# Kernel tuning notes

Hardware: AMD Instinct MI355X
Metric: run time of the kernel (lower is better)

The kernel has to match this reference:

```python
import jax, jax.numpy as jnp
import numpy as np

NEG_SLOPE = 0.2
EPS = 1e-16
HEADS1, OUT1 = 4, 32
HEADS2, OUT2 = 1, 32


def _gat_conv(x, W, a_src, a_dst, bias, src, dst, num_nodes, heads, out_c, concat):
    # x: [N, F_in], W: [F_in, heads*out_c], a_*: [heads, out_c]
    h = (x @ W).reshape(num_nodes, heads, out_c)            # [N, H, C]
    alpha_src = (h * a_src).sum(-1)                          # [N, H]
    alpha_dst = (h * a_dst).sum(-1)                          # [N, H]
    e = jax.nn.leaky_relu(alpha_src[src] + alpha_dst[dst], NEG_SLOPE)  # [E, H]
    # softmax over incoming edges of each destination node (PyG softmax)
    m = jax.ops.segment_max(e, dst, num_segments=num_nodes)
    ex = jnp.exp(e - m[dst])
    s = jax.ops.segment_sum(ex, dst, num_segments=num_nodes)
    alpha = ex / (s[dst] + EPS)                              # [E, H]
    out = jax.ops.segment_sum(h[src] * alpha[:, :, None], dst,
                              num_segments=num_nodes)        # [N, H, C]
    out = out.reshape(num_nodes, heads * out_c) if concat else out.mean(axis=1)
    return out + bias


def setup_inputs() -> dict:
    key = jax.random.key(0)
    ks = jax.random.split(key, 10)
    N, E, F_IN = 50000, 1600000, 128
    sc = 0.1
    return {
        "x": jax.random.normal(ks[0], (N, F_IN), jnp.float32),
        "edge_index": jax.random.randint(ks[1], (2, E), 0, N, jnp.int32),
        "W1": jax.random.normal(ks[2], (F_IN, HEADS1 * OUT1), jnp.float32) * sc,
        "a_src1": jax.random.normal(ks[3], (HEADS1, OUT1), jnp.float32) * sc,
        "a_dst1": jax.random.normal(ks[4], (HEADS1, OUT1), jnp.float32) * sc,
        "b1": jax.random.normal(ks[5], (HEADS1 * OUT1,), jnp.float32) * sc,
        "W2": jax.random.normal(ks[6], (HEADS1 * OUT1, HEADS2 * OUT2), jnp.float32) * sc,
        "a_src2": jax.random.normal(ks[7], (HEADS2, OUT2), jnp.float32) * sc,
        "a_dst2": jax.random.normal(ks[8], (HEADS2, OUT2), jnp.float32) * sc,
        "b2": jax.random.normal(ks[9], (OUT2,), jnp.float32) * sc,
    }


def reference(x, edge_index, W1, a_src1, a_dst1, b1, W2, a_src2, a_dst2, b2):
    N = x.shape[0]
    # PyG GATConv default add_self_loops=True
    loops = jnp.arange(N, dtype=edge_index.dtype)
    src = jnp.concatenate([edge_index[0], loops])
    dst = jnp.concatenate([edge_index[1], loops])
    h = _gat_conv(x, W1, a_src1, a_dst1, b1, src, dst, N, HEADS1, OUT1, True)
    h = jax.nn.elu(h)
    return _gat_conv(h, W2, a_src2, a_dst2, b2, src, dst, N, HEADS2, OUT2, False)
```

## Files before the change

### kernel.cpp

```cpp
#include <hip/hip_runtime.h>
#include <math.h>

#define NEG_SLOPE 0.2f
#define EPSV 1e-16f
#define NPART 4

typedef _Float16 half4 __attribute__((ext_vector_type(4)));
typedef _Float16 half8 __attribute__((ext_vector_type(8)));
typedef float floatx2 __attribute__((ext_vector_type(2)));


__global__ void k_scan_blk(const int* __restrict__ degp, int N,
                           int* __restrict__ rowptr, int* __restrict__ bsum){
    int b = blockIdx.x, t = threadIdx.x;
    int base = b * 1024 + t * 4;
    int v[4];
    #pragma unroll
    for (int j = 0; j < 4; j++){
        int n = base + j, s = 0;
        if (n < N){
            #pragma unroll
            for (int p = 0; p < NPART; p++) s += degp[p * N + n];
        }
        v[j] = s;
    }
    int s = v[0] + v[1] + v[2] + v[3];
    int lane = t & 63, wid = t >> 6;
    int x = s;
    #pragma unroll
    for (int off = 1; off < 64; off <<= 1){
        int y = __shfl_up(x, off, 64);
        if (lane >= off) x += y;
    }
    __shared__ int ws[4];
    if (lane == 63) ws[wid] = x;
    __syncthreads();
    int woff = 0;
    for (int w = 0; w < wid; w++) woff += ws[w];
    int run = woff + x - s;
    #pragma unroll
    for (int j = 0; j < 4; j++){
        if (base + j < N) rowptr[base + j] = run;
        run += v[j];
    }
    if (t == 255) bsum[b] = woff + x;
}

__global__ void k_finalize(const int* __restrict__ bsum, const int* __restrict__ degp,
                           int N, int ET,
                           int* __restrict__ rowptr, int* __restrict__ poff){
    int b = blockIdx.x, t = threadIdx.x;
    int n = b * 256 + t;
    int chunk = (b * 256) >> 10;
    int off = 0;
    for (int c = 0; c < chunk; c++) off += bsum[c];
    if (n < N){
        int r = rowptr[n] + off;
        rowptr[n] = r;
        int run = r;
        #pragma unroll
        for (int p = 0; p < NPART; p++){
            poff[p * N + n] = run;
            run += degp[p * N + n];
        }
    }
    if (n == 0) rowptr[N] = ET;
}

__launch_bounds__(256)
__global__ void k_scatter2(const int* __restrict__ ei, int E, int ET, int N,
                           const int* __restrict__ poff,
                           const unsigned short* __restrict__ rank,
                           int* __restrict__ csr_src){
    int i = blockIdx.x * 256 + threadIdx.x;
    if (i >= ET) return;
    int s, d;
    if (i < E){ s = ei[i]; d = ei[E + i]; } else { s = i - E; d = s; }
    int p = (i >> 8) & (NPART - 1);
    csr_src[poff[p * N + d] + (int)rank[i]] = s;
}


__launch_bounds__(256)
__global__ void k_gemm1_hist(const float* __restrict__ x, const float* __restrict__ W1,
                             const float* __restrict__ a_src, const float* __restrict__ a_dst,
                             _Float16* __restrict__ h1h, float* __restrict__ asrc1,
                             float* __restrict__ adst1, int N, int nGemmBlk,
                             const int* __restrict__ ei, int E, int ET,
                             int* __restrict__ degp, unsigned short* __restrict__ rank){
    __shared__ float Wl[16 * 128];
    __shared__ float xl[32 * 128];
    int t = threadIdx.x;
    if ((int)blockIdx.x >= nGemmBlk){
        int base = (blockIdx.x - nGemmBlk) * 1024 + t;
        #pragma unroll
        for (int j = 0; j < 4; j++){
            int i = base + j * 256;
            if (i < ET){
                int d = (i < E) ? ei[E + i] : (i - E);
                int p = (i >> 8) & (NPART - 1);
                rank[i] = (unsigned short)atomicAdd(&degp[p * N + d], 1);
            }
        }
        return;
    }
    int cg = t & 31, ns = t >> 5;
    int n0 = blockIdx.x * 32;
    for (int idx = t; idx < 1024; idx += 256){
        int row = idx >> 5, k4 = idx & 31;
        float4 v = {0.f, 0.f, 0.f, 0.f};
        if (n0 + row < N) v = *(const float4*)&x[(size_t)(n0 + row) * 128 + k4 * 4];
        *(float4*)&xl[row * 128 + k4 * 4] = v;
    }
    float4 acc0 = {0,0,0,0}, acc1 = {0,0,0,0}, acc2 = {0,0,0,0}, acc3 = {0,0,0,0};
    for (int c = 0; c < 8; c++){
        __syncthreads();
        for (int idx = t; idx < 512; idx += 256)
            *(float4*)&Wl[idx * 4] = *(const float4*)&W1[c * 16 * 128 + idx * 4];
        __syncthreads();
        #pragma unroll
        for (int k = 0; k < 16; k += 4){
            float4 xv0 = *(float4*)&xl[(ns     ) * 128 + c * 16 + k];
            float4 xv1 = *(float4*)&xl[(ns +  8) * 128 + c * 16 + k];
            float4 xv2 = *(float4*)&xl[(ns + 16) * 128 + c * 16 + k];
            float4 xv3 = *(float4*)&xl[(ns + 24) * 128 + c * 16 + k];
            #pragma unroll
            for (int kk = 0; kk < 4; kk++){
                float4 w = *(float4*)&Wl[(k + kk) * 128 + cg * 4];
                float x0 = ((float*)&xv0)[kk];
                float x1 = ((float*)&xv1)[kk];
                float x2v= ((float*)&xv2)[kk];
                float x3 = ((float*)&xv3)[kk];
                acc0.x = fmaf(x0, w.x, acc0.x); acc0.y = fmaf(x0, w.y, acc0.y);
                acc0.z = fmaf(x0, w.z, acc0.z); acc0.w = fmaf(x0, w.w, acc0.w);
                acc1.x = fmaf(x1, w.x, acc1.x); acc1.y = fmaf(x1, w.y, acc1.y);
                acc1.z = fmaf(x1, w.z, acc1.z); acc1.w = fmaf(x1, w.w, acc1.w);
                acc2.x = fmaf(x2v, w.x, acc2.x); acc2.y = fmaf(x2v, w.y, acc2.y);
                acc2.z = fmaf(x2v, w.z, acc2.z); acc2.w = fmaf(x2v, w.w, acc2.w);
                acc3.x = fmaf(x3, w.x, acc3.x); acc3.y = fmaf(x3, w.y, acc3.y);
                acc3.z = fmaf(x3, w.z, acc3.z); acc3.w = fmaf(x3, w.w, acc3.w);
            }
        }
    }
    float4 a4s = *(const float4*)&a_src[cg * 4];
    float4 a4d = *(const float4*)&a_dst[cg * 4];
    float4 accs[4] = {acc0, acc1, acc2, acc3};
    #pragma unroll
    for (int j = 0; j < 4; j++){
        int n = n0 + ns + 8 * j;
        if (n >= N) continue;
        float4 a = accs[j];
        half4 hv;
        hv.x = (_Float16)a.x; hv.y = (_Float16)a.y;
        hv.z = (_Float16)a.z; hv.w = (_Float16)a.w;
        *(half4*)&h1h[((size_t)n << 7) + (cg << 2)] = hv;
        float vs = a.x * a4s.x + a.y * a4s.y + a.z * a4s.z + a.w * a4s.w;
        float vd = a.x * a4d.x + a.y * a4d.y + a.z * a4d.z + a.w * a4d.w;
        #pragma unroll
        for (int m = 1; m <= 4; m <<= 1){
            vs += __shfl_xor(vs, m, 64);
            vd += __shfl_xor(vd, m, 64);
        }
        if ((cg & 7) == 0){
            int head = cg >> 3;
            asrc1[n * 4 + head] = vs;
            adst1[n * 4 + head] = vd;
        }
    }
}


__launch_bounds__(256)
__global__ void k_agg1(const int* __restrict__ rowptr, const int* __restrict__ csr_src,
                       const float* __restrict__ asrc1, const float* __restrict__ adst1,
                       const _Float16* __restrict__ h1h,
                       const float* __restrict__ b1, float* __restrict__ x2){
    int t = threadIdx.x;
    int n = blockIdx.x * 4 + (t >> 6);
    int lane = t & 63, g = lane >> 4, l = lane & 15, head = l >> 2;
    int start = rowptr[n], end = rowptr[n + 1];
    float adn = adst1[(n << 2) + head];
    const char* hb = (const char*)h1h;
    const char* ab = (const char*)asrc1;
    int hoff = l << 4;
    int aoff = head << 2;
    floatx2 rA[4], rB[4];
    #pragma unroll
    for (int j = 0; j < 4; j++){ rA[j] = (floatx2)0.f; rB[j] = (floatx2)0.f; }
    float sA = 0.f, sB = 0.f;
    int i = start + g;
    for (; i + 4 < end; i += 8){
        int s0 = csr_src[i];
        int s1 = csr_src[i + 4];
        float e0 = *(const float*)(ab + (s0 << 4) + aoff) + adn;
        float e1 = *(const float*)(ab + (s1 << 4) + aoff) + adn;
        e0 = fmaxf(e0, NEG_SLOPE * e0);
        e1 = fmaxf(e1, NEG_SLOPE * e1);
        float w0 = __expf(e0);
        float w1 = __expf(e1);
        half8 h0 = *(const half8*)(hb + (s0 << 8) + hoff);
        half8 h1v = *(const half8*)(hb + (s1 << 8) + hoff);
        sA += w0; sB += w1;
        floatx2 w02 = {w0, w0}, w12 = {w1, w1};
        #pragma unroll
        for (int j = 0; j < 4; j++){
            floatx2 c0 = {(float)h0[2*j], (float)h0[2*j+1]};
            floatx2 c1 = {(float)h1v[2*j], (float)h1v[2*j+1]};
            rA[j] = w02 * c0 + rA[j];
            rB[j] = w12 * c1 + rB[j];
        }
    }
    if (i < end){
        int s0 = csr_src[i];
        float e0 = *(const float*)(ab + (s0 << 4) + aoff) + adn;
        e0 = fmaxf(e0, NEG_SLOPE * e0);
        float w0 = __expf(e0);
        half8 h0 = *(const half8*)(hb + (s0 << 8) + hoff);
        sA += w0;
        floatx2 w02 = {w0, w0};
        #pragma unroll
        for (int j = 0; j < 4; j++){
            floatx2 c0 = {(float)h0[2*j], (float)h0[2*j+1]};
            rA[j] = w02 * c0 + rA[j];
        }
    }
    float r[9];
    #pragma unroll
    for (int j = 0; j < 4; j++){
        floatx2 c = rA[j] + rB[j];
        r[2*j] = c.x; r[2*j+1] = c.y;
    }
    r[8] = sA + sB;
    #pragma unroll
    for (int m = 16; m <= 32; m <<= 1)
        #pragma unroll
        for (int j = 0; j < 9; j++) r[j] += __shfl_xor(r[j], m, 64);
    if (g == 0){
        float inv = 1.f / (r[8] + EPSV);
        float o[8];
        #pragma unroll
        for (int j = 0; j < 8; j++){
            float v = r[j] * inv + b1[l * 8 + j];
            o[j] = (v > 0.f) ? v : expm1f(v);
        }
        float4 o0 = {o[0], o[1], o[2], o[3]};
        float4 o1 = {o[4], o[5], o[6], o[7]};
        *(float4*)&x2[((size_t)n << 7) + (l << 3)]     = o0;
        *(float4*)&x2[((size_t)n << 7) + (l << 3) + 4] = o1;
    }
}


__launch_bounds__(256)
__global__ void k_gemm2(const float* __restrict__ x2, const float* __restrict__ W2,
                        const float* __restrict__ a_src, const float* __restrict__ a_dst,
                        _Float16* __restrict__ h2h, float* __restrict__ asrc2,
                        float* __restrict__ adst2, int N){
    __shared__ float Wl[128 * 32];
    __shared__ float xl[64 * 128];
    int t = threadIdx.x;
    int cg = t & 7, ns = t >> 3;
    for (int idx = t; idx < 1024; idx += 256)
        *(float4*)&Wl[idx * 4] = *(const float4*)&W2[idx * 4];
    int n0 = blockIdx.x * 64;
    for (int idx = t; idx < 2048; idx += 256){
        int row = idx >> 5, k4 = idx & 31;
        float4 v = {0.f, 0.f, 0.f, 0.f};
        if (n0 + row < N) v = *(const float4*)&x2[(size_t)(n0 + row) * 128 + k4 * 4];
        *(float4*)&xl[row * 128 + k4 * 4] = v;
    }
    __syncthreads();
    float4 acc0 = {0,0,0,0}, acc1 = {0,0,0,0};
    #pragma unroll 2
    for (int k = 0; k < 128; k += 4){
        float4 xv0 = *(float4*)&xl[(ns      ) * 128 + k];
        float4 xv1 = *(float4*)&xl[(ns + 32) * 128 + k];
        #pragma unroll
        for (int kk = 0; kk < 4; kk++){
            float4 w = *(float4*)&Wl[(k + kk) * 32 + cg * 4];
            float x0 = ((float*)&xv0)[kk];
            float x1 = ((float*)&xv1)[kk];
            acc0.x = fmaf(x0, w.x, acc0.x); acc0.y = fmaf(x0, w.y, acc0.y);
            acc0.z = fmaf(x0, w.z, acc0.z); acc0.w = fmaf(x0, w.w, acc0.w);
            acc1.x = fmaf(x1, w.x, acc1.x); acc1.y = fmaf(x1, w.y, acc1.y);
            acc1.z = fmaf(x1, w.z, acc1.z); acc1.w = fmaf(x1, w.w, acc1.w);
        }
    }
    float4 a4s = *(const float4*)&a_src[cg * 4];
    float4 a4d = *(const float4*)&a_dst[cg * 4];
    float4 accs[2] = {acc0, acc1};
    #pragma unroll
    for (int j = 0; j < 2; j++){
        int n = n0 + ns + 32 * j;
        if (n >= N) continue;
        float4 a = accs[j];
        half4 hv;
        hv.x = (_Float16)a.x; hv.y = (_Float16)a.y;
        hv.z = (_Float16)a.z; hv.w = (_Float16)a.w;
        *(half4*)&h2h[((size_t)n << 5) + (cg << 2)] = hv;
        float vs = a.x * a4s.x + a.y * a4s.y + a.z * a4s.z + a.w * a4s.w;
        float vd = a.x * a4d.x + a.y * a4d.y + a.z * a4d.z + a.w * a4d.w;
        #pragma unroll
        for (int m = 1; m <= 4; m <<= 1){
            vs += __shfl_xor(vs, m, 64);
            vd += __shfl_xor(vd, m, 64);
        }
        if (cg == 0){ asrc2[n] = vs; adst2[n] = vd; }
    }
}


__launch_bounds__(256)
__global__ void k_agg2(const int* __restrict__ rowptr, const int* __restrict__ csr_src,
                       const float* __restrict__ asrc2, const float* __restrict__ adst2,
                       const _Float16* __restrict__ h2h,
                       const float* __restrict__ b2, float* __restrict__ out){
    int t = threadIdx.x;
    int n = blockIdx.x * 8 + (t >> 5);
    int l5 = t & 31, g = l5 >> 3, l = l5 & 7;
    int start = rowptr[n], end = rowptr[n + 1];
    float adn = adst2[n];
    const char* hb = (const char*)h2h;
    const char* ab = (const char*)asrc2;
    int hoff = l << 3;
    floatx2 aA[2], aB[2];
    aA[0] = (floatx2)0.f; aA[1] = (floatx2)0.f;
    aB[0] = (floatx2)0.f; aB[1] = (floatx2)0.f;
    float sA = 0.f, sB = 0.f;
    int i = start + g;
    for (; i + 4 < end; i += 8){
        int s0 = csr_src[i];
        int s1 = csr_src[i + 4];
        float e0 = *(const float*)(ab + (s0 << 2)) + adn;
        float e1 = *(const float*)(ab + (s1 << 2)) + adn;
        e0 = fmaxf(e0, NEG_SLOPE * e0);
        e1 = fmaxf(e1, NEG_SLOPE * e1);
        float w0 = __expf(e0);
        float w1 = __expf(e1);
        half4 h0 = *(const half4*)(hb + (s0 << 6) + hoff);
        half4 h1v = *(const half4*)(hb + (s1 << 6) + hoff);
        sA += w0; sB += w1;
        floatx2 w02 = {w0, w0}, w12 = {w1, w1};
        floatx2 c00 = {(float)h0.x, (float)h0.y}, c01 = {(float)h0.z, (float)h0.w};
        floatx2 c10 = {(float)h1v.x, (float)h1v.y}, c11 = {(float)h1v.z, (float)h1v.w};
        aA[0] = w02 * c00 + aA[0]; aA[1] = w02 * c01 + aA[1];
        aB[0] = w12 * c10 + aB[0]; aB[1] = w12 * c11 + aB[1];
    }
    if (i < end){
        int s0 = csr_src[i];
        float e0 = *(const float*)(ab + (s0 << 2)) + adn;
        e0 = fmaxf(e0, NEG_SLOPE * e0);
        float w0 = __expf(e0);
        half4 h0 = *(const half4*)(hb + (s0 << 6) + hoff);
        sA += w0;
        floatx2 w02 = {w0, w0};
        floatx2 c00 = {(float)h0.x, (float)h0.y}, c01 = {(float)h0.z, (float)h0.w};
        aA[0] = w02 * c00 + aA[0]; aA[1] = w02 * c01 + aA[1];
    }
    floatx2 m0 = aA[0] + aB[0], m1 = aA[1] + aB[1];
    float4 acc = {m0.x, m0.y, m1.x, m1.y};
    float ssum = sA + sB;
    #pragma unroll
    for (int m = 8; m <= 16; m <<= 1){
        acc.x += __shfl_xor(acc.x, m, 64);
        acc.y += __shfl_xor(acc.y, m, 64);
        acc.z += __shfl_xor(acc.z, m, 64);
        acc.w += __shfl_xor(acc.w, m, 64);
        ssum  += __shfl_xor(ssum,  m, 64);
    }
    if (g == 0){
        float inv = 1.f / (ssum + EPSV);
        const float4 b4 = *(const float4*)&b2[l * 4];
        float4 o;
        o.x = acc.x * inv + b4.x; o.y = acc.y * inv + b4.y;
        o.z = acc.z * inv + b4.z; o.w = acc.w * inv + b4.w;
        *(float4*)&out[((size_t)n << 5) + l * 4] = o;
    }
}


extern "C" void kernel_launch(void* const* d_in, const int* in_sizes, int n_in,
                              void* d_out, int out_size, void* d_ws, size_t ws_size,
                              hipStream_t stream){
    const float* x      = (const float*)d_in[0];
    const int*   ei     = (const int*)  d_in[1];
    const float* W1     = (const float*)d_in[2];
    const float* a_src1 = (const float*)d_in[3];
    const float* a_dst1 = (const float*)d_in[4];
    const float* b1     = (const float*)d_in[5];
    const float* W2     = (const float*)d_in[6];
    const float* a_src2 = (const float*)d_in[7];
    const float* a_dst2 = (const float*)d_in[8];
    const float* b2     = (const float*)d_in[9];
    float* out = (float*)d_out;

    int N  = in_sizes[0] / 128;
    int E  = in_sizes[1] / 2;
    int ET = E + N;
    int nScanBlk = (N + 1023) / 1024;
    int G  = (ET + 255) / 256;
    int GH = (ET + 1023) / 1024;
    int nGemmBlk = (N + 31) / 32;

    char* ws = (char*)d_ws;
    size_t off = 0;
    auto alloc = [&](size_t bytes) -> char* {
        char* p = ws + off;
        off += (bytes + 255) & ~(size_t)255;
        return p;
    };
    int*            degp    = (int*)           alloc((size_t)NPART * N * 4);
    int*            rowptr  = (int*)           alloc((size_t)(N + 1) * 4);
    int*            bsum    = (int*)           alloc((size_t)nScanBlk * 4);
    unsigned short* rank    = (unsigned short*)alloc((size_t)ET * 2);
    int*            poff    = (int*)           alloc((size_t)NPART * N * 4);
    int*            csr_src = (int*)           alloc((size_t)ET * 4);
    _Float16*       h1h     = (_Float16*)      alloc((size_t)N * 128 * 2);
    float*          x2      = (float*)         alloc((size_t)N * 128 * 4);
    float*          asrc1   = (float*)         alloc((size_t)N * 4 * 4);
    float*          adst1   = (float*)         alloc((size_t)N * 4 * 4);
    _Float16*       h2h     = (_Float16*)      alloc((size_t)N * 32 * 2);
    float*          asrc2   = (float*)         alloc((size_t)N * 4);
    float*          adst2   = (float*)         alloc((size_t)N * 4);

    hipMemsetAsync(degp, 0, (size_t)NPART * N * 4, stream);
    hipLaunchKernelGGL(k_gemm1_hist, dim3(nGemmBlk + GH), dim3(256), 0, stream,
                       x, W1, a_src1, a_dst1, h1h, asrc1, adst1, N, nGemmBlk,
                       ei, E, ET, degp, rank);
    hipLaunchKernelGGL(k_scan_blk,  dim3(nScanBlk), dim3(256), 0, stream, degp, N, rowptr, bsum);
    hipLaunchKernelGGL(k_finalize,  dim3((N + 255) / 256), dim3(256), 0, stream, bsum, degp, N, ET, rowptr, poff);
    hipLaunchKernelGGL(k_scatter2,  dim3(G), dim3(256), 0, stream, ei, E, ET, N, poff, rank, csr_src);
    hipLaunchKernelGGL(k_agg1,      dim3(N / 4), dim3(256), 0, stream, rowptr, csr_src, asrc1, adst1, h1h, b1, x2);
    hipLaunchKernelGGL(k_gemm2,     dim3((N + 63) / 64), dim3(256), 0, stream, x2, W2, a_src2, a_dst2, h2h, asrc2, adst2, N);
    hipLaunchKernelGGL(k_agg2,      dim3(N / 8), dim3(256), 0, stream, rowptr, csr_src, asrc2, adst2, h2h, b2, out);
}
```

Baseline: 303.8 us.

## Partition degree histogram by XCC, enlarge GEMM1 tile and keep W in registers

The degree-histogram atomics now pick their partition from the hardware XCC id read via s_getreg, with NPART raised to 8. The partition is packed into the high bits of the 16-bit rank so the scatter can recover it, which limits per-partition degree to 8191. The atomics use workgroup scope, relying on each partition being touched only from one XCC. GEMM1 now computes 64 rows per block with 8 accumulators and loads W1 straight from global into registers instead of staging it in LDS, dropping the per-chunk barriers. The goal is less cross-die atomic contention and fewer LDS round trips, at the cost of higher register pressure.

```diff
diff --git a/kernel.cpp b/kernel.cpp
--- a/kernel.cpp
+++ b/kernel.cpp
@@ -3,7 +3,7 @@
 
 #define NEG_SLOPE 0.2f
 #define EPSV 1e-16f
-#define NPART 4
+#define NPART 8
 
 typedef _Float16 half4 __attribute__((ext_vector_type(4)));
 typedef _Float16 half8 __attribute__((ext_vector_type(8)));
@@ -76,80 +76,80 @@
     if (i >= ET) return;
     int s, d;
     if (i < E){ s = ei[i]; d = ei[E + i]; } else { s = i - E; d = s; }
-    int p = (i >> 8) & (NPART - 1);
-    csr_src[poff[p * N + d] + (int)rank[i]] = s;
-}
-
-
-__launch_bounds__(256)
+    int pr = rank[i];
+    int p = pr >> 13, r = pr & 0x1FFF;
+    csr_src[poff[p * N + d] + r] = s;
+}
+
+
+__launch_bounds__(256, 3)
 __global__ void k_gemm1_hist(const float* __restrict__ x, const float* __restrict__ W1,
                              const float* __restrict__ a_src, const float* __restrict__ a_dst,
                              _Float16* __restrict__ h1h, float* __restrict__ asrc1,
                              float* __restrict__ adst1, int N, int nGemmBlk,
                              const int* __restrict__ ei, int E, int ET,
-                             int* __restrict__ degp, unsigned short* __restrict__ rank){
-    __shared__ float Wl[16 * 128];
-    __shared__ float xl[32 * 128];
+                             unsigned int* __restrict__ degp, unsigned short* __restrict__ rank){
+    __shared__ float xl[64 * 128];
     int t = threadIdx.x;
     if ((int)blockIdx.x >= nGemmBlk){
+        int p = __builtin_amdgcn_s_getreg((3 << 11) | 20) & 7;
         int base = (blockIdx.x - nGemmBlk) * 1024 + t;
         #pragma unroll
         for (int j = 0; j < 4; j++){
             int i = base + j * 256;
             if (i < ET){
                 int d = (i < E) ? ei[E + i] : (i - E);
-                int p = (i >> 8) & (NPART - 1);
-                rank[i] = (unsigned short)atomicAdd(&degp[p * N + d], 1);
+                unsigned r = __hip_atomic_fetch_add(&degp[(size_t)p * N + d], 1u,
+                                 __ATOMIC_RELAXED, __HIP_MEMORY_SCOPE_WORKGROUP);
+                rank[i] = (unsigned short)((p << 13) | r);
             }
         }
         return;
     }
-    int cg = t & 31, ns = t >> 5;
-    int n0 = blockIdx.x * 32;
-    for (int idx = t; idx < 1024; idx += 256){
+    int cg = t & 31, rs = t >> 5;
+    int n0 = blockIdx.x * 64;
+    for (int idx = t; idx < 2048; idx += 256){
         int row = idx >> 5, k4 = idx & 31;
         float4 v = {0.f, 0.f, 0.f, 0.f};
         if (n0 + row < N) v = *(const float4*)&x[(size_t)(n0 + row) * 128 + k4 * 4];
         *(float4*)&xl[row * 128 + k4 * 4] = v;
     }
-    float4 acc0 = {0,0,0,0}, acc1 = {0,0,0,0}, acc2 = {0,0,0,0}, acc3 = {0,0,0,0};
-    for (int c = 0; c < 8; c++){
-        __syncthreads();
-        for (int idx = t; idx < 512; idx += 256)
-            *(float4*)&Wl[idx * 4] = *(const float4*)&W1[c * 16 * 128 + idx * 4];
-        __syncthreads();
-        #pragma unroll
-        for (int k = 0; k < 16; k += 4){
-            float4 xv0 = *(float4*)&xl[(ns     ) * 128 + c * 16 + k];
-            float4 xv1 = *(float4*)&xl[(ns +  8) * 128 + c * 16 + k];
-            float4 xv2 = *(float4*)&xl[(ns + 16) * 128 + c * 16 + k];
-            float4 xv3 = *(float4*)&xl[(ns + 24) * 128 + c * 16 + k];
+    __syncthreads();
+    float4 acc[8];
+    #pragma unroll
+    for (int j = 0; j < 8; j++) acc[j] = (float4){0.f, 0.f, 0.f, 0.f};
+    for (int hc = 0; hc < 16; hc++){
+        float4 wr[8];
+        #pragma unroll
+        for (int k = 0; k < 8; k++)
+            wr[k] = *(const float4*)&W1[(hc * 8 + k) * 128 + cg * 4];
+        #pragma unroll
+        for (int kb = 0; kb < 8; kb += 4){
+            float4 xv[8];
+            #pragma unroll
+            for (int j = 0; j < 8; j++)
+                xv[j] = *(const float4*)&xl[(rs + 8 * j) * 128 + hc * 8 + kb];
             #pragma unroll
             for (int kk = 0; kk < 4; kk++){
-                float4 w = *(float4*)&Wl[(k + kk) * 128 + cg * 4];
-                float x0 = ((float*)&xv0)[kk];
-                float x1 = ((float*)&xv1)[kk];
-                float x2v= ((float*)&xv2)[kk];
-                float x3 = ((float*)&xv3)[kk];
-                acc0.x = fmaf(x0, w.x, acc0.x); acc0.y = fmaf(x0, w.y, acc0.y);
-                acc0.z = fmaf(x0, w.z, acc0.z); acc0.w = fmaf(x0, w.w, acc0.w);
-                acc1.x = fmaf(x1, w.x, acc1.x); acc1.y = fmaf(x1, w.y, acc1.y);
-                acc1.z = fmaf(x1, w.z, acc1.z); acc1.w = fmaf(x1, w.w, acc1.w);
-                acc2.x = fmaf(x2v, w.x, acc2.x); acc2.y = fmaf(x2v, w.y, acc2.y);
-                acc2.z = fmaf(x2v, w.z, acc2.z); acc2.w = fmaf(x2v, w.w, acc2.w);
-                acc3.x = fmaf(x3, w.x, acc3.x); acc3.y = fmaf(x3, w.y, acc3.y);
-                acc3.z = fmaf(x3, w.z, acc3.z); acc3.w = fmaf(x3, w.w, acc3.w);
+                float4 w = wr[kb + kk];
+                #pragma unroll
+                for (int j = 0; j < 8; j++){
+                    float xs = ((const float*)&xv[j])[kk];
+                    acc[j].x = fmaf(xs, w.x, acc[j].x);
+                    acc[j].y = fmaf(xs, w.y, acc[j].y);
+                    acc[j].z = fmaf(xs, w.z, acc[j].z);
+                    acc[j].w = fmaf(xs, w.w, acc[j].w);
+                }
             }
         }
     }
     float4 a4s = *(const float4*)&a_src[cg * 4];
     float4 a4d = *(const float4*)&a_dst[cg * 4];
-    float4 accs[4] = {acc0, acc1, acc2, acc3};
-    #pragma unroll
-    for (int j = 0; j < 4; j++){
-        int n = n0 + ns + 8 * j;
+    #pragma unroll
+    for (int j = 0; j < 8; j++){
+        int n = n0 + rs + 8 * j;
         if (n >= N) continue;
-        float4 a = accs[j];
+        float4 a = acc[j];
         half4 hv;
         hv.x = (_Float16)a.x; hv.y = (_Float16)a.y;
         hv.z = (_Float16)a.z; hv.w = (_Float16)a.w;
@@ -400,7 +400,7 @@
     int nScanBlk = (N + 1023) / 1024;
     int G  = (ET + 255) / 256;
     int GH = (ET + 1023) / 1024;
-    int nGemmBlk = (N + 31) / 32;
+    int nGemmBlk = (N + 63) / 64;
 
     char* ws = (char*)d_ws;
     size_t off = 0;
@@ -426,7 +426,7 @@
     hipMemsetAsync(degp, 0, (size_t)NPART * N * 4, stream);
     hipLaunchKernelGGL(k_gemm1_hist, dim3(nGemmBlk + GH), dim3(256), 0, stream,
                        x, W1, a_src1, a_dst1, h1h, asrc1, adst1, N, nGemmBlk,
-                       ei, E, ET, degp, rank);
+                       ei, E, ET, (unsigned int*)degp, rank);
     hipLaunchKernelGGL(k_scan_blk,  dim3(nScanBlk), dim3(256), 0, stream, degp, N, rowptr, bsum);
     hipLaunchKernelGGL(k_finalize,  dim3((N + 255) / 256), dim3(256), 0, stream, bsum, degp, N, ET, rowptr, poff);
     hipLaunchKernelGGL(k_scatter2,  dim3(G), dim3(256), 0, stream, ei, E, ET, N, poff, rank, csr_src);
```

New measurement: 299.8 us. Within noise of the previous version (-1.3%).
